# Kernel optimization log

Hardware: AMD Instinct MI355X
Metric: run time of the kernel (lower is better)

## Reference

```python
import jax, jax.numpy as jnp
import numpy as np

# ---- static config (matches init_kwargs) ----
R, A, K = 2048, 4, 4          # residues, backbone atoms, neighborhood size (self + <=3 edges)
N, B, C = R * A, 8, 64        # nodes, batch, hidden dim (= num_channels+time_embedding_channels)
H, D = 4, 16                  # heads, dim_head
HD, L = H * D, 4              # heads*dim_head, depth
E, Tc = 128, 61               # time_embedding_dim, time_embedding_channels
EPS = 1e-6


def _build_neighbors():
    """Fixed-K neighbor lists from the protein-backbone adjacency (self at k=0)."""
    adj = [[] for _ in range(N)]
    for r in range(R):
        b = r * A
        edges = [(b, b + 1), (b + 1, b + 2), (b + 2, b + 3)]
        if r < R - 1:
            edges.append((b + 2, (r + 1) * A))
        for i, j in edges:
            adj[i].append(j)
            adj[j].append(i)
    nbr = np.zeros((N, K), np.int32)
    msk = np.zeros((N, K), bool)
    for i in range(N):
        nbr[i, 0] = i
        msk[i, 0] = True
        for k, j in enumerate(adj[i][:K - 1]):
            nbr[i, k + 1] = j
            msk[i, k + 1] = True
    return jnp.asarray(nbr), jnp.asarray(msk)


def setup_inputs() -> dict:
    key = jax.random.key(0)
    ks = jax.random.split(key, 24)
    nbr, msk = _build_neighbors()

    def rn(i, shape, scale=1.0):
        return jax.random.normal(ks[i], shape, dtype=jnp.float32) * scale

    return {
        "x": rn(0, (B, N, 3)),
        "y": rn(1, (B, N, 3)),  # present in forward signature, unused by the math
        "t": jax.random.uniform(ks[2], (B,), dtype=jnp.float32),
        "nbr_idx": nbr, "nbr_mask": msk,
        "t_w1": rn(3, (E, E), E ** -0.5), "t_b1": jnp.zeros((E,), jnp.float32),
        "t_w2": rn(4, (E, Tc), E ** -0.5), "t_b2": jnp.zeros((Tc,), jnp.float32),
        "win1": rn(5, (C,)),
        "Wq0": rn(6, (L, C, HD), C ** -0.5), "Wk0": rn(7, (L, C, HD), C ** -0.5), "Wv0": rn(8, (L, C, HD), C ** -0.5),
        "Wq1": rn(9, (L, C, HD), C ** -0.5), "Wk1": rn(10, (L, C, HD), C ** -0.5), "Wv1": rn(11, (L, C, HD), C ** -0.5),
        "Wo0": rn(12, (L, HD, C), HD ** -0.5), "Wo1": rn(13, (L, HD, C), HD ** -0.5),
        "Wff0a": rn(14, (L, C, 4 * C), C ** -0.5), "Wff0b": rn(15, (L, 4 * C, C), (4 * C) ** -0.5),
        "Wff1": rn(16, (L, C, C), C ** -0.5),
        "Wout": rn(17, (3, C), C ** -0.5), "bout": jnp.zeros((3,), jnp.float32),
    }


def _sin_embed(t):
    half = E // 2
    freqs = jnp.exp(-jnp.log(10000.0) * jnp.arange(half, dtype=jnp.float32) / half)
    emb = t[:, None] * freqs
    return jnp.concatenate([jnp.sin(emb), jnp.cos(emb)], axis=-1)


def _ln(x):  # layernorm over channels, no affine
    mu = x.mean(-1, keepdims=True)
    v = x.var(-1, keepdims=True)
    return (x - mu) * jax.lax.rsqrt(v + EPS)


def _vnorm(f1):  # equivariant norm: scale by RMS of per-channel vector norms
    sq = jnp.sum(f1 * f1, axis=-1)                                    # [B,N,C]
    s = jax.lax.rsqrt(jnp.mean(sq, axis=-1, keepdims=True) + EPS)     # [B,N,1]
    return f1 * s[..., None]


def reference(x, y, t, nbr_idx, nbr_mask, t_w1, t_b1, t_w2, t_b2, win1,
              Wq0, Wk0, Wv0, Wq1, Wk1, Wv1, Wo0, Wo1, Wff0a, Wff0b, Wff1,
              Wout, bout):
    # time embedding MLP
    te = _sin_embed(t)
    te = jax.nn.silu(te @ t_w1 + t_b1) @ t_w2 + t_b2                  # [B,Tc]
    # degree-0 input: time embedding broadcast to nodes, concat positions
    f0 = jnp.concatenate([jnp.broadcast_to(te[:, None, :], (B, N, Tc)), x], axis=-1)  # [B,N,C]
    # degree-1 input: single vector channel (positions), lifted to C channels
    f1 = jnp.einsum('bnv,c->bncv', x, win1)                           # [B,N,C,3]

    rel = x[:, nbr_idx] - x[:, :, None, :]                            # [B,N,K,3]
    rhat = rel * jax.lax.rsqrt(jnp.sum(rel * rel, -1, keepdims=True) + EPS)
    mbias = jnp.where(nbr_mask, 0.0, -1e9)[None, :, None, :]          # [1,N,1,K]
    scale = D ** -0.5

    for l in range(L):
        g0, g1 = _ln(f0), _vnorm(f1)
        g0j = g0[:, nbr_idx]                                          # [B,N,K,C]
        g1j = g1[:, nbr_idx]                                          # [B,N,K,C,3]
        q0 = jnp.einsum('bnc,ce->bne', g0, Wq0[l]).reshape(B, N, H, D)
        k0 = jnp.einsum('bnkc,ce->bnke', g0j, Wk0[l]).reshape(B, N, K, H, D)
        v0 = jnp.einsum('bnkc,ce->bnke', g0j, Wv0[l]).reshape(B, N, K, H, D)
        q1 = jnp.einsum('bncv,ce->bnev', g1, Wq1[l]).reshape(B, N, H, D, 3)
        k1 = jnp.einsum('bnkcv,ce->bnkev', g1j, Wk1[l]).reshape(B, N, K, H, D, 3)
        v1 = jnp.einsum('bnkcv,ce->bnkev', g1j, Wv1[l]).reshape(B, N, K, H, D, 3)
        logits = (jnp.einsum('bnhd,bnkhd->bnhk', q0, k0)
                  + jnp.einsum('bnhdv,bnkhdv->bnhk', q1, k1)) * scale + mbias
        a = jax.nn.softmax(logits, axis=-1)                           # [B,N,H,K]
        # degree-mixing tensor products along edge direction rhat
        v1to0 = jnp.einsum('bnkhdv,bnkv->bnkhd', v1, rhat)            # 1 -> 0
        v0to1 = v0[..., None] * rhat[:, :, :, None, None, :]          # 0 -> 1
        o0 = jnp.einsum('bnhk,bnkhd->bnhd', a, v0 + v1to0).reshape(B, N, HD)
        o1 = jnp.einsum('bnhk,bnkhdv->bnhdv', a, v1 + v0to1).reshape(B, N, HD, 3)
        f0 = f0 + o0 @ Wo0[l]
        f1 = f1 + jnp.einsum('bnev,ec->bncv', o1, Wo1[l])
        # feedforward (equivariant: vector branch is linear in channels)
        f0 = f0 + jax.nn.silu(_ln(f0) @ Wff0a[l]) @ Wff0b[l]
        f1 = f1 + jnp.einsum('bncv,ce->bnev', _vnorm(f1), Wff1[l])

    # output layer: per-component channel projection of the degree-1 features
    score = jnp.einsum('bncv,vc->bnv', f1, Wout) + bout               # [B,N,3]
    return score
```

## Files before the change

### kernel.cpp

```cpp
#include <hip/hip_runtime.h>

#define BB 8
#define NN 8192
#define RR 2048
#define LL 4
#define TC 61
#define EPSF 1e-6f
#define BN (BB*NN)
#define OUTN (BN*3)

typedef unsigned short u16;
typedef unsigned int u32;
typedef _Float16 h2f __attribute__((ext_vector_type(2)));
typedef _Float16 h8 __attribute__((ext_vector_type(8)));
typedef float f4 __attribute__((ext_vector_type(4)));

__device__ __forceinline__ u32 packf16(float a, float b) {
  h2f h; h.x = (_Float16)a; h.y = (_Float16)b; return __builtin_bit_cast(u32, h);
}
__device__ __forceinline__ u16 f16b(float a) {
  _Float16 h = (_Float16)a; return __builtin_bit_cast(u16, h);
}
__device__ __forceinline__ float2 unpk(u32 a) {
  h2f h = __builtin_bit_cast(h2f, a); return make_float2((float)h.x, (float)h.y);
}
__device__ __forceinline__ float fdot2(u32 a, u32 b, float c) {
  return __builtin_amdgcn_fdot2(__builtin_bit_cast(h2f, a), __builtin_bit_cast(h2f, b), c, false);
}
__device__ __forceinline__ float frcp(float x) { return __builtin_amdgcn_rcpf(x); }
__device__ __forceinline__ float frsq(float x) { return __builtin_amdgcn_rsqf(x); }
__device__ __forceinline__ float fexp(float x) { return __expf(x); }
__device__ __forceinline__ int kmax_of(int n) {
  int aatom = n & 3, rres = n >> 2;
  return (aatom==0) ? (rres==0 ? 2 : 3)
       : (aatom==1) ? 3
       : (aatom==2) ? (rres==RR-1 ? 3 : 4) : 2;
}

__global__ __launch_bounds__(256) void k_const(float* out, float v) {
  int i = blockIdx.x*256 + threadIdx.x;
  if (i < OUTN) out[i] = v;
}

struct WSrc { const float* m[11]; };
__global__ __launch_bounds__(256) void k_prep(WSrc s, u32* W16,
    const float* t, const float* w1, const float* b1,
    const float* w2, const float* b2, float* te2,
    const float* x, const int* nbr, u16* rhat) {
  if (blockIdx.x >= 1096) {
    int i = (blockIdx.x - 1096)*256 + threadIdx.x;
    int tok = i >> 2, k = i & 3;
    int b = tok >> 13, n = tok & (NN-1);
    int tj = b*NN + nbr[n*4 + k];
    float x0 = x[tok*3+0], x1 = x[tok*3+1], x2 = x[tok*3+2];
    float rx = x[tj*3+0] - x0, ry = x[tj*3+1] - x1, rz = x[tj*3+2] - x2;
    float ir = rsqrtf(rx*rx + ry*ry + rz*rz + EPSF);
    rhat[(size_t)(tok*4+k)*3 + 0] = f16b(rx * ir);
    rhat[(size_t)(tok*4+k)*3 + 1] = f16b(ry * ir);
    rhat[(size_t)(tok*4+k)*3 + 2] = f16b(rz * ir);
    return;
  }
  if (blockIdx.x >= 1088) {
    __shared__ float s0[128], s1[128];
    int bb = blockIdx.x - 1088;
    int j = threadIdx.x;
    float tv = t[bb];
    if (j < 128) {
      int i = j & 63;
      float fr = expf(-9.210340371976184f * (float)i * (1.0f/64.0f));
      float em = tv * fr;
      s0[j] = (j < 64) ? sinf(em) : cosf(em);
    }
    __syncthreads();
    if (j < 128) {
      float acc = b1[j];
      for (int i2 = 0; i2 < 128; ++i2) acc += s0[i2] * w1[i2*128 + j];
      s1[j] = acc / (1.f + expf(-acc));
    }
    __syncthreads();
    if (j < TC) {
      float a2 = b2[j];
      for (int i2 = 0; i2 < 128; ++i2) a2 += s1[i2] * w2[i2*TC + j];
      te2[bb*TC + j] = a2;
    }
    return;
  }
  int i = blockIdx.x*256 + threadIdx.x;
  if (i < 73728) {
    int m = i >> 13, rr = i & 8191, l = rr >> 11, r2 = rr & 2047;
    int c2 = r2 >> 6, col = r2 & 63;
    const float* src = s.m[m] + l*4096;
    W16[i] = packf16(src[(2*c2)*64 + col], src[(2*c2+1)*64 + col]);
  } else if (i < 106496) {
    int j2 = i - 73728; int l = j2 >> 13, r2 = j2 & 8191;
    int c2 = r2 >> 8, j = r2 & 255;
    const float* src = s.m[9] + l*16384;
    W16[i] = packf16(src[(2*c2)*256 + j], src[(2*c2+1)*256 + j]);
  } else if (i < 139264) {
    int j2 = i - 106496; int l = j2 >> 13, r2 = j2 & 8191;
    int jp = r2 >> 6, e = r2 & 63;
    const float* src = s.m[10] + l*16384;
    W16[i] = packf16(src[(2*jp)*64 + e], src[(2*jp+1)*64 + e]);
  } else if (i < 188416) {
    int j2 = i - 139264;
    int l = j2 / 12288, rem = j2 % 12288;
    int m = rem >> 11, r2 = rem & 2047;
    int fb = r2 >> 8, li = r2 & 255;
    int nt = fb >> 1, kc = fb & 1;
    int lane = li >> 2, j = li & 3;
    int c2 = kc*16 + (lane>>4)*4 + j;
    int e  = nt*16 + (lane & 15);
    const float* src = s.m[m] + l*4096;
    W16[i] = packf16(src[(2*c2)*64 + e], src[(2*c2+1)*64 + e]);
  } else {
    int j2 = i - 188416;
    int l = j2 / 22528, rem = j2 % 22528;
    int li, fb, msel, N;
    const float* srcb;
    if (rem < 6144) {
      msel = 6 + (rem >> 11);
      int r2 = rem & 2047;
      fb = r2 >> 8; li = r2 & 255;
      srcb = s.m[msel] + l*4096; N = 64;
      int nt = fb >> 1, kc = fb & 1;
      int lane = li >> 2, j = li & 3;
      int c2 = kc*16 + (lane>>4)*4 + j;
      int e  = nt*16 + (lane & 15);
      W16[i] = packf16(srcb[(2*c2)*N + e], srcb[(2*c2+1)*N + e]);
    } else if (rem < 14336) {
      int r2 = rem - 6144;
      fb = r2 >> 8; li = r2 & 255;
      srcb = s.m[9] + l*16384; N = 256;
      int nt = fb >> 1, kc = fb & 1;
      int lane = li >> 2, j = li & 3;
      int c2 = kc*16 + (lane>>4)*4 + j;
      int e  = nt*16 + (lane & 15);
      W16[i] = packf16(srcb[(2*c2)*N + e], srcb[(2*c2+1)*N + e]);
    } else {
      int r2 = rem - 14336;
      fb = r2 >> 8; li = r2 & 255;
      srcb = s.m[10] + l*16384; N = 64;
      int nt = fb >> 3, kc = fb & 7;
      int lane = li >> 2, j = li & 3;
      int c2 = kc*16 + (lane>>4)*4 + j;
      int e  = nt*16 + (lane & 15);
      W16[i] = packf16(srcb[(2*c2)*N + e], srcb[(2*c2+1)*N + e]);
    }
  }
}

#define QH  0
#define KRG 4352
#define LK0 (KRG)
#define LV0 (KRG+1152)
#define LK1 (KRG+2304)
#define LV1 (KRG+5760)
#define LO0 (KRG)
#define LO1 (KRG+1152)
#define LVN (KRG+4608)
#define LGG (KRG+8064)
#define LDSU 13568

__global__ __launch_bounds__(256, 3) void k_layer(const u32* __restrict__ W16, int l,
    const u32* __restrict__ f0i, const u32* __restrict__ f1i,
    const int* __restrict__ nbr, const u16* __restrict__ rhat,
    u32* __restrict__ f0o, u32* __restrict__ f1o,
    const float* __restrict__ wout, const float* __restrict__ bout,
    float* __restrict__ out,
    const float* __restrict__ x, const float* __restrict__ win1,
    const float* __restrict__ te2) {
  __shared__ __align__(16) u32 S[LDSU];
  int tid = threadIdx.x, wv = tid >> 6, lane = tid & 63;
  int arow = lane & 15, aq = lane >> 4;
  int t0g = blockIdx.x * 32;
  int b = t0g >> 13, n0 = t0g & (NN-1);
  const u32 ONE2 = 0x3C003C00u;

  uint4 res0, res1a, res1b, res1c;
  if (l == 0) {
    {
      int t0 = tid >> 3, j0 = (tid & 7)*4;
      const float* x3 = x + ((size_t)b*NN + n0 + t0)*3;
      float xv[3] = {x3[0], x3[1], x3[2]};
      u32 tmp[4];
#pragma unroll
      for (int q = 0; q < 4; ++q) {
        int ca = 2*(j0+q), cb = ca+1;
        float va = (ca < TC) ? te2[b*TC+ca] : xv[ca-61];
        float vb = (cb < TC) ? te2[b*TC+cb] : xv[cb-61];
        tmp[q] = packf16(va, vb);
      }
      res0 = make_uint4(tmp[0], tmp[1], tmp[2], tmp[3]);
    }
    uint4* rr[3] = {&res1a, &res1b, &res1c};
#pragma unroll
    for (int k = 0; k < 3; ++k) {
      int idx = k*1024 + tid*4;
      int t = idx/96, rem = idx%96, v = rem >> 5, j = rem & 31;
      float xv = x[((size_t)b*NN + n0 + t)*3 + v];
      u32 tmp[4];
#pragma unroll
      for (int q = 0; q < 4; ++q)
        tmp[q] = packf16(xv*win1[2*(j+q)], xv*win1[2*(j+q)+1]);
      *rr[k] = make_uint4(tmp[0], tmp[1], tmp[2], tmp[3]);
    }
  } else {
    const u32* s0 = f0i + ((size_t)b*NN + n0)*32;
    const u32* s1 = f1i + ((size_t)b*NN + n0)*96;
    res0  = *(const uint4*)(s0 + tid*4);
    res1a = *(const uint4*)(s1 + (0*256 + tid)*4);
    res1b = *(const uint4*)(s1 + (1*256 + tid)*4);
    res1c = *(const uint4*)(s1 + (2*256 + tid)*4);
  }

  {
    const u32* base = W16 + 139264 + l*12288;
    int ncol = arow, mb = aq*4;

    auto ldraw = [&](int hr0, u32* r0, u32 (*r1)[8]) {
      int n = n0 - 2 + hr0 + arow;
      n = n < 0 ? 0 : (n > NN-1 ? NN-1 : n);
      size_t gt = (size_t)b*NN + n;
      if (l == 0) {
        const float* x3 = x + gt*3;
        float xv[3] = {x3[0], x3[1], x3[2]};
#pragma unroll
        for (int i = 0; i < 8; ++i) {
          int j = (i < 4) ? (aq*4+i) : (16 + aq*4 + (i-4));
          int ca = 2*j, cb = ca+1;
          float va = (ca < TC) ? te2[b*TC+ca] : xv[ca-61];
          float vb = (cb < TC) ? te2[b*TC+cb] : xv[cb-61];
          r0[i] = packf16(va, vb);
          float wa = win1[ca], wb = win1[cb];
#pragma unroll
          for (int v = 0; v < 3; ++v)
            r1[v][i] = packf16(xv[v]*wa, xv[v]*wb);
        }
      } else {
        *(uint4*)(r0)   = *(const uint4*)(f0i + gt*32 + aq*4);
        *(uint4*)(r0+4) = *(const uint4*)(f0i + gt*32 + 16 + aq*4);
#pragma unroll
        for (int v = 0; v < 3; ++v) {
          *(uint4*)(r1[v])   = *(const uint4*)(f1i + (gt*3+v)*32 + aq*4);
          *(uint4*)(r1[v]+4) = *(const uint4*)(f1i + (gt*3+v)*32 + 16 + aq*4);
        }
      }
    };

    auto mknorm = [&](const u32* r0, const u32 (*r1)[8], h8* g0f, h8 (*g1f)[2]) {
      float s = 0.f, s2 = 0.f;
#pragma unroll
      for (int i = 0; i < 8; ++i) { s = fdot2(r0[i], ONE2, s); s2 = fdot2(r0[i], r0[i], s2); }
      s  += __shfl_xor(s, 16, 64);  s  += __shfl_xor(s, 32, 64);
      s2 += __shfl_xor(s2, 16, 64); s2 += __shfl_xor(s2, 32, 64);
      float mu = s*(1.f/64.f);
      float ri = frsq(fmaxf(s2*(1.f/64.f)-mu*mu, 0.f) + EPSF);
      _Float16 rih = (_Float16)ri, bih = (_Float16)(-mu*ri);
      h2f scv; scv.x = rih; scv.y = rih;
      h2f biv; biv.x = bih; biv.y = bih;
#pragma unroll
      for (int kc = 0; kc < 2; ++kc) {
        u32 t0[4];
#pragma unroll
        for (int i = 0; i < 4; ++i) {
          h2f g = __builtin_bit_cast(h2f, r0[kc*4+i]) * scv + biv;
          t0[i] = __builtin_bit_cast(u32, g);
        }
        g0f[kc] = __builtin_bit_cast(h8, make_uint4(t0[0], t0[1], t0[2], t0[3]));
      }
      float ss = 0.f;
#pragma unroll
      for (int v = 0; v < 3; ++v)
#pragma unroll
        for (int i = 0; i < 8; ++i) ss = fdot2(r1[v][i], r1[v][i], ss);
      ss += __shfl_xor(ss, 16, 64); ss += __shfl_xor(ss, 32, 64);
      float vs = frsq(ss*(1.f/64.f) + EPSF);
      _Float16 vsh = (_Float16)vs;
      h2f vsv; vsv.x = vsh; vsv.y = vsh;
#pragma unroll
      for (int v = 0; v < 3; ++v)
#pragma unroll
        for (int kc = 0; kc < 2; ++kc) {
          u32 t1[4];
#pragma unroll
          for (int i = 0; i < 4; ++i) {
            h2f g = __builtin_bit_cast(h2f, r1[v][kc*4+i]) * vsv;
            t1[i] = __builtin_bit_cast(u32, g);
          }
          g1f[v][kc] = __builtin_bit_cast(h8, make_uint4(t1[0], t1[1], t1[2], t1[3]));
        }
    };

    auto projs = [&](const h8* afr, const u32* wM, u16* outh, int ob, int rmax) {
#pragma unroll
      for (int nt = 0; nt < 4; ++nt) {
        f4 acc = {0.f, 0.f, 0.f, 0.f};
#pragma unroll
        for (int kc = 0; kc < 2; ++kc) {
          uint4 wb = *(const uint4*)(wM + (nt*2+kc)*256 + lane*4);
          acc = __builtin_amdgcn_mfma_f32_16x16x32_f16(afr[kc], __builtin_bit_cast(h8, wb), acc, 0, 0, 0);
        }
        int ex = ((nt ^ aq)&3)*16 + ncol;
#pragma unroll
        for (int r = 0; r < 4; ++r) {
          int orow = ob + mb + r;
          if (orow < rmax) outh[orow*64 + ex] = f16b(acc[r]);
        }
      }
    };

    h8 g0f[2]; h8 g1f[3][2];
    if (wv < 3) {
      int tb = wv*16;
      u32 r0[8]; u32 r1[3][8];
      ldraw(tb, r0, r1);
      mknorm(r0, r1, g0f, g1f);
      projs(g0f, base + 1*2048, (u16*)(S+LK0), tb, 36);
      projs(g0f, base + 2*2048, (u16*)(S+LV0), tb, 36);
#pragma unroll
      for (int v = 0; v < 3; ++v) {
        projs(g1f[v], base + 4*2048, (u16*)(S+LK1) + v*2304, tb, 36);
        projs(g1f[v], base + 5*2048, (u16*)(S+LV1) + v*2304, tb, 36);
      }
    } else {
      u32 r0a[8], r1a[3][8], r0b[8], r1b[3][8];
      ldraw(2, r0a, r1a);
      ldraw(18, r0b, r1b);
      mknorm(r0a, r1a, g0f, g1f);
      projs(g0f, base, (u16*)(S+QH), 0, 32);
#pragma unroll
      for (int v = 0; v < 3; ++v)
        projs(g1f[v], base + 3*2048, (u16*)(S+1024) + v*2048, 0, 32);
      mknorm(r0b, r1b, g0f, g1f);
      projs(g0f, base, (u16*)(S+QH), 16, 32);
#pragma unroll
      for (int v = 0; v < 3; ++v)
        projs(g1f[v], base + 3*2048, (u16*)(S+1024) + v*2048, 16, 32);
    }
  }
  __syncthreads();

  u32 O0k[4], O1k[4][3];
  {
    const u32* Q0u = S + QH;
    const u32* Q1u = S + 1024;
    const u32* K0u = S + LK0;
    const u32* V0u = S + LV0;
    const u32* K1u = S + LK1;
    const u32* V1u = S + LV1;
    int half = lane >> 5, l32 = lane & 31;
#pragma unroll
    for (int it = 0; it < 4; ++it) {
      int ct = wv*8 + it*2 + half;
      int n = n0 + ct;
      size_t gt = (size_t)b*NN + n;
      int km = kmax_of(n);
      int4 nb = *(const int4*)(nbr + n*4);
      int lr[4];
      {
        int xx;
        xx = nb.x - n0 + 2; lr[0] = xx < 0 ? 0 : (xx > 35 ? 35 : xx);
        xx = nb.y - n0 + 2; lr[1] = xx < 0 ? 0 : (xx > 35 ? 35 : xx);
        xx = nb.z - n0 + 2; lr[2] = xx < 0 ? 0 : (xx > 35 ? 35 : xx);
        xx = nb.w - n0 + 2; lr[3] = xx < 0 ? 0 : (xx > 35 ? 35 : xx);
      }
      int jq = l32 ^ (((ct>>2)&3)<<3);
      u32 q0p = Q0u[ct*32 + jq];
      u32 q1p[3];
#pragma unroll
      for (int v = 0; v < 3; ++v) q1p[v] = Q1u[v*1024 + ct*32 + jq];
      float p[4];
#pragma unroll
      for (int k = 0; k < 4; ++k) {
        int row = lr[k];
        int jk = l32 ^ (((row>>2)&3)<<3);
        float acc = fdot2(q0p, K0u[row*32 + jk], 0.f);
#pragma unroll
        for (int v = 0; v < 3; ++v)
          acc = fdot2(q1p[v], K1u[v*1152 + row*32 + jk], acc);
        p[k] = acc;
      }
#pragma unroll
      for (int m = 1; m < 8; m <<= 1) {
#pragma unroll
        for (int k = 0; k < 4; ++k) p[k] += __shfl_xor(p[k], m, 64);
      }
      float mx = -1e30f;
#pragma unroll
      for (int k = 0; k < 4; ++k) { p[k] *= 0.25f; if (k < km) mx = fmaxf(mx, p[k]); }
      float aw[4], ssum = 0.f;
#pragma unroll
      for (int k = 0; k < 4; ++k) { aw[k] = (k < km) ? fexp(p[k]-mx) : 0.f; ssum += aw[k]; }
      float inv = frcp(ssum);
      const uint2* rp = (const uint2*)(rhat + (size_t)gt*12);
      uint2 ra = rp[0], rb = rp[1], rc = rp[2];
      u32 rw[6] = {ra.x, ra.y, rb.x, rb.y, rc.x, rc.y};
      h2f o0p = {(_Float16)0.f, (_Float16)0.f};
      h2f o1p0 = o0p, o1p1 = o0p, o1p2 = o0p;
#pragma unroll
      for (int k = 0; k < 4; ++k) {
        int row = lr[k];
        int jk = l32 ^ (((row>>2)&3)<<3);
        float a = aw[k]*inv;
        _Float16 ah = (_Float16)a;
        h2f a2; a2.x = ah; a2.y = ah;
        h2f v0p = __builtin_bit_cast(h2f, V0u[row*32 + jk]);
        h2f v1p[3], rh2[3];
#pragma unroll
        for (int v = 0; v < 3; ++v) {
          v1p[v] = __builtin_bit_cast(h2f, V1u[v*1152 + row*32 + jk]);
          int idx = k*3 + v;
          u32 w = rw[idx>>1];
          u32 hh = (idx&1) ? (w >> 16) : (w & 0xffffu);
          rh2[v] = __builtin_bit_cast(h2f, (hh << 16) | hh);
        }
        h2f vd = v1p[0]*rh2[0];
        vd = v1p[1]*rh2[1] + vd;
        vd = v1p[2]*rh2[2] + vd;
        o0p  = a2*(v0p + vd) + o0p;
        o1p0 = a2*(v0p*rh2[0] + v1p[0]) + o1p0;
        o1p1 = a2*(v0p*rh2[1] + v1p[1]) + o1p1;
        o1p2 = a2*(v0p*rh2[2] + v1p[2]) + o1p2;
      }
      O0k[it] = __builtin_bit_cast(u32, o0p);
      O1k[it][0] = __builtin_bit_cast(u32, o1p0);
      O1k[it][1] = __builtin_bit_cast(u32, o1p1);
      O1k[it][2] = __builtin_bit_cast(u32, o1p2);
    }
  }
  __syncthreads();

  {
    u32* o0u = S + LO0;
    u32* o1u = S + LO1;
    int half = lane >> 5, l32 = lane & 31;
#pragma unroll
    for (int it = 0; it < 4; ++it) {
      int ct = wv*8 + it*2 + half;
      o0u[ct*36 + l32] = O0k[it];
#pragma unroll
      for (int v = 0; v < 3; ++v)
        o1u[(v*32+ct)*36 + l32] = O1k[it][v];
    }
  }
  __syncthreads();

  int tl16 = (wv & 1)*16;
  h8 a1[3][2]; h8 a0[2];
  if (wv < 2) {
#pragma unroll
    for (int v = 0; v < 3; ++v)
#pragma unroll
      for (int kc = 0; kc < 2; ++kc)
        a1[v][kc] = __builtin_bit_cast(h8, *(const uint4*)(S + LO1 + (v*32 + tl16 + arow)*36 + kc*16 + aq*4));
  } else {
#pragma unroll
    for (int kc = 0; kc < 2; ++kc)
      a0[kc] = __builtin_bit_cast(h8, *(const uint4*)(S + LO0 + (tl16 + arow)*36 + kc*16 + aq*4));
  }
  __syncthreads();
  {
    uint4* d = (uint4*)(S + KRG);
    d[tid]       = res0;
    d[256 + tid] = res1a;
    d[512 + tid] = res1b;
    d[768 + tid] = res1c;
  }
  __syncthreads();
  const u32* FR0 = S + KRG;
  const u32* FR1 = S + KRG + 1024;

  {
    int ncol = arow, mb = aq*4;
    const u32* Wf = W16 + 188416 + l*22528;
    const u32* po0f = Wf;
    const u32* po1f = Wf + 2048;
    const u32* pf1f = Wf + 4096;
    const u32* paf  = Wf + 6144;
    const u32* pbf  = Wf + 14336;
    size_t gt0 = (size_t)b*NN + n0 + tl16;
    if (wv < 2) {
      float f1m[3][4][4];
#pragma unroll
      for (int v = 0; v < 3; ++v)
#pragma unroll
        for (int nt = 0; nt < 4; ++nt) {
          f4 acc = {0.f, 0.f, 0.f, 0.f};
#pragma unroll
          for (int kc = 0; kc < 2; ++kc) {
            uint4 wb = *(const uint4*)(po1f + (nt*2+kc)*256 + lane*4);
            acc = __builtin_amdgcn_mfma_f32_16x16x32_f16(a1[v][kc], __builtin_bit_cast(h8, wb), acc, 0, 0, 0);
          }
#pragma unroll
          for (int r = 0; r < 4; ++r) {
            int t = tl16 + mb + r;
            float2 pq = unpk(FR1[(t*3+v)*32 + nt*8 + (ncol>>1)]);
            f1m[v][nt][r] = acc[r] + ((ncol&1) ? pq.y : pq.x);
          }
        }
      float vs[4];
#pragma unroll
      for (int r = 0; r < 4; ++r) {
        float ss = 0.f;
#pragma unroll
        for (int v = 0; v < 3; ++v)
#pragma unroll
          for (int nt = 0; nt < 4; ++nt) ss += f1m[v][nt][r]*f1m[v][nt][r];
        ss += __shfl_xor(ss, 1, 64); ss += __shfl_xor(ss, 2, 64);
        ss += __shfl_xor(ss, 4, 64); ss += __shfl_xor(ss, 8, 64);
        vs[r] = frsq(ss*(1.f/64.f) + EPSF);
      }
      u32* vn = S + LVN + wv*1728;
      {
        u16* vnh = (u16*)vn;
#pragma unroll
        for (int v = 0; v < 3; ++v)
#pragma unroll
          for (int nt = 0; nt < 4; ++nt)
#pragma unroll
            for (int r = 0; r < 4; ++r)
              vnh[v*1152 + (mb+r)*72 + nt*16 + ncol] = f16b(f1m[v][nt][r]*vs[r]);
      }
      float wl[3][4], sc[3][4];
      if (l == 3) {
#pragma unroll
        for (int v = 0; v < 3; ++v)
#pragma unroll
          for (int nt = 0; nt < 4; ++nt) { wl[v][nt] = wout[v*64 + nt*16 + ncol]; }
#pragma unroll
        for (int v = 0; v < 3; ++v)
#pragma unroll
          for (int r = 0; r < 4; ++r) sc[v][r] = 0.f;
      }
#pragma unroll
      for (int v = 0; v < 3; ++v)
#pragma unroll
        for (int nt = 0; nt < 4; ++nt) {
          f4 acc = {0.f, 0.f, 0.f, 0.f};
#pragma unroll
          for (int kc = 0; kc < 2; ++kc) {
            h8 af = __builtin_bit_cast(h8, *(const uint4*)(vn + v*576 + arow*36 + kc*16 + aq*4));
            uint4 wb = *(const uint4*)(pf1f + (nt*2+kc)*256 + lane*4);
            acc = __builtin_amdgcn_mfma_f32_16x16x32_f16(af, __builtin_bit_cast(h8, wb), acc, 0, 0, 0);
          }
#pragma unroll
          for (int r = 0; r < 4; ++r) {
            size_t gt = gt0 + mb + r;
            float val = acc[r] + f1m[v][nt][r];
            if (l < 3) {
              float par = __shfl_xor(val, 1, 64);
              if (!(ncol & 1))
                f1o[(gt*3+v)*32 + nt*8 + (ncol>>1)] = packf16(val, par);
            } else {
              sc[v][r] += val * wl[v][nt];
            }
          }
        }
      if (l == 3) {
#pragma unroll
        for (int v = 0; v < 3; ++v)
#pragma unroll
          for (int r = 0; r < 4; ++r) {
            float xx = sc[v][r];
            xx += __shfl_xor(xx, 1, 64); xx += __shfl_xor(xx, 2, 64);
            xx += __shfl_xor(xx, 4, 64); xx += __shfl_xor(xx, 8, 64);
            if (ncol == 0) out[(gt0 + mb + r)*3 + v] = xx + bout[v];
          }
      }
    } else if (l < 3) {
      float f0m[4][4];
#pragma unroll
      for (int nt = 0; nt < 4; ++nt) {
        f4 acc = {0.f, 0.f, 0.f, 0.f};
#pragma unroll
        for (int kc = 0; kc < 2; ++kc) {
          uint4 wb = *(const uint4*)(po0f + (nt*2+kc)*256 + lane*4);
          acc = __builtin_amdgcn_mfma_f32_16x16x32_f16(a0[kc], __builtin_bit_cast(h8, wb), acc, 0, 0, 0);
        }
#pragma unroll
        for (int r = 0; r < 4; ++r) {
          int t = tl16 + mb + r;
          float2 pq = unpk(FR0[t*32 + nt*8 + (ncol>>1)]);
          f0m[nt][r] = acc[r] + ((ncol&1) ? pq.y : pq.x);
        }
      }
      float mu[4], ri[4];
#pragma unroll
      for (int r = 0; r < 4; ++r) {
        float sg = 0.f, s2 = 0.f;
#pragma unroll
        for (int nt = 0; nt < 4; ++nt) { sg += f0m[nt][r]; s2 += f0m[nt][r]*f0m[nt][r]; }
        sg += __shfl_xor(sg, 1, 64); sg += __shfl_xor(sg, 2, 64);
        sg += __shfl_xor(sg, 4, 64); sg += __shfl_xor(sg, 8, 64);
        s2 += __shfl_xor(s2, 1, 64); s2 += __shfl_xor(s2, 2, 64);
        s2 += __shfl_xor(s2, 4, 64); s2 += __shfl_xor(s2, 8, 64);
        mu[r] = sg*(1.f/64.f);
        ri[r] = frsq(fmaxf(s2*(1.f/64.f)-mu[r]*mu[r], 0.f) + EPSF);
      }
      u32* gg = S + LGG + (wv-2)*576;
      {
        u16* gh = (u16*)gg;
#pragma unroll
        for (int nt = 0; nt < 4; ++nt)
#pragma unroll
          for (int r = 0; r < 4; ++r)
            gh[(mb+r)*72 + nt*16 + ncol] = f16b((f0m[nt][r]-mu[r])*ri[r]);
      }
      u32* hp = S + (wv-2)*2176;
      {
        h8 ga[2];
#pragma unroll
        for (int kc = 0; kc < 2; ++kc)
          ga[kc] = __builtin_bit_cast(h8, *(const uint4*)(gg + arow*36 + kc*16 + aq*4));
        u16* hhh = (u16*)hp;
#pragma unroll
        for (int nt16 = 0; nt16 < 16; ++nt16) {
          f4 acc = {0.f, 0.f, 0.f, 0.f};
#pragma unroll
          for (int kc = 0; kc < 2; ++kc) {
            uint4 wb = *(const uint4*)(paf + (nt16*2+kc)*256 + lane*4);
            acc = __builtin_amdgcn_mfma_f32_16x16x32_f16(ga[kc], __builtin_bit_cast(h8, wb), acc, 0, 0, 0);
          }
#pragma unroll
          for (int r = 0; r < 4; ++r) {
            float a = acc[r];
            hhh[(mb+r)*272 + nt16*16 + ncol] = f16b(a * frcp(1.f + fexp(-a)));
          }
        }
      }
#pragma unroll
      for (int nt = 0; nt < 4; ++nt) {
        f4 acc = {0.f, 0.f, 0.f, 0.f};
#pragma unroll
        for (int kc = 0; kc < 8; ++kc) {
          h8 af = __builtin_bit_cast(h8, *(const uint4*)(hp + arow*136 + kc*16 + aq*4));
          uint4 wb = *(const uint4*)(pbf + (nt*8+kc)*256 + lane*4);
          acc = __builtin_amdgcn_mfma_f32_16x16x32_f16(af, __builtin_bit_cast(h8, wb), acc, 0, 0, 0);
        }
#pragma unroll
        for (int r = 0; r < 4; ++r) {
          size_t gt = gt0 + mb + r;
          float val = acc[r] + f0m[nt][r];
          float par = __shfl_xor(val, 1, 64);
          if (!(ncol & 1))
            f0o[gt*32 + nt*8 + (ncol>>1)] = packf16(val, par);
        }
      }
    }
  }
}

extern "C" void kernel_launch(void* const* d_in, const int* in_sizes, int n_in,
                              void* d_out, int out_size, void* d_ws, size_t ws_size,
                              hipStream_t stream) {
  float* out = (float*)d_out;
  static const int exp23[23] = {196608,196608,8,32768,32768,16384,128,7808,61,64,
                                16384,16384,16384,16384,16384,16384,16384,16384,
                                65536,65536,16384,192,3};
  bool ok23 = (n_in == 23), ok22 = (n_in == 22);
  int bad = -1;
  if (ok23) {
    for (int i = 0; i < 23; ++i) if (in_sizes[i] != exp23[i]) { ok23 = false; bad = i; break; }
  }
  if (!ok23 && ok22) {
    for (int i = 0; i < 22; ++i) {
      int want = (i == 0) ? exp23[0] : exp23[i+1];
      if (in_sizes[i] != want) { ok22 = false; if (bad < 0) bad = i; break; }
    }
  } else ok22 = false;
  if (!ok23 && !ok22) {
    k_const<<<768, 256, 0, stream>>>(out, (float)(3000 + (bad < 0 ? 100 + n_in : bad)));
    return;
  }
  int sh = ok23 ? 0 : -1;
  const int* nbr = (const int*)d_in[3 + sh];
  const float* F[20];
  F[0] = (const float*)d_in[0];
  F[1] = (const float*)d_in[2 + sh];
  for (int j = 0; j < 18; ++j) F[2 + j] = (const float*)d_in[5 + sh + j];

  char* ws = (char*)d_ws;
  u32*   W16  = (u32*)ws;
  float* te2  = (float*)(ws + 1114112);
  u16*   rhat = (u16*)(ws + 1116160);
  u32*   f0A  = (u32*)(ws + 2689024);
  u32*   f1A  = (u32*)(ws + 11077632);
  u32*   f0B  = (u32*)(ws + 36243456);
  u32*   f1B  = (u32*)(ws + 44632064);

  WSrc s;
  s.m[0]=F[7]; s.m[1]=F[8]; s.m[2]=F[9]; s.m[3]=F[10]; s.m[4]=F[11]; s.m[5]=F[12];
  s.m[6]=F[13]; s.m[7]=F[14]; s.m[8]=F[17]; s.m[9]=F[15]; s.m[10]=F[16];

  k_prep<<<1096 + BN*4/256, 256, 0, stream>>>(s, W16, F[1], F[2], F[3], F[4], F[5], te2,
                                              F[0], nbr, rhat);
  for (int l = 0; l < LL; ++l) {
    const u32* fi0 = (l & 1) ? f0B : f0A;
    const u32* fi1 = (l & 1) ? f1B : f1A;
    u32*       fo0 = (l & 1) ? f0A : f0B;
    u32*       fo1 = (l & 1) ? f1A : f1B;
    k_layer<<<BN/32, 256, 0, stream>>>(W16, l, fi0, fi1, nbr, rhat, fo0, fo1,
                                       F[18], F[19], out, F[0], F[6], te2);
  }
}
```

Baseline: 377.8 us.

## Merge residual staging with output stores and swizzle LDS scratch to drop barriers

The residual registers are now written to shared memory alongside the attention outputs, before a single barrier. Each wave then loads its MFMA operands directly, which removes two __syncthreads and a separate staging pass. The vector-norm and layer-norm scratch tiles now reuse each wave's own residual region, with an XOR-swizzled unpadded layout in place of padded rows. This relies on each wave reading its residual slice before overwriting it with scratch data, which holds because the wave runs in lockstep.

```diff
diff --git a/kernel.cpp b/kernel.cpp
--- a/kernel.cpp
+++ b/kernel.cpp
@@ -155,10 +155,10 @@
 #define LV0 (KRG+1152)
 #define LK1 (KRG+2304)
 #define LV1 (KRG+5760)
-#define LO0 (KRG)
-#define LO1 (KRG+1152)
-#define LVN (KRG+4608)
-#define LGG (KRG+8064)
+#define LO0q (KRG)
+#define LO1q (KRG+1152)
+#define FR0q (KRG+4608)
+#define FR1q (KRG+5632)
 #define LDSU 13568
 
 __global__ __launch_bounds__(256, 3) void k_layer(const u32* __restrict__ W16, int l,
@@ -431,8 +431,8 @@
   __syncthreads();
 
   {
-    u32* o0u = S + LO0;
-    u32* o1u = S + LO1;
+    u32* o0u = S + LO0q;
+    u32* o1u = S + LO1q;
     int half = lane >> 5, l32 = lane & 31;
 #pragma unroll
     for (int it = 0; it < 4; ++it) {
@@ -442,35 +442,17 @@
       for (int v = 0; v < 3; ++v)
         o1u[(v*32+ct)*36 + l32] = O1k[it][v];
     }
+    uint4* d0 = (uint4*)(S + FR0q);
+    d0[tid] = res0;
+    uint4* d1 = (uint4*)(S + FR1q);
+    d1[tid]       = res1a;
+    d1[256 + tid] = res1b;
+    d1[512 + tid] = res1c;
   }
   __syncthreads();
 
-  int tl16 = (wv & 1)*16;
-  h8 a1[3][2]; h8 a0[2];
-  if (wv < 2) {
-#pragma unroll
-    for (int v = 0; v < 3; ++v)
-#pragma unroll
-      for (int kc = 0; kc < 2; ++kc)
-        a1[v][kc] = __builtin_bit_cast(h8, *(const uint4*)(S + LO1 + (v*32 + tl16 + arow)*36 + kc*16 + aq*4));
-  } else {
-#pragma unroll
-    for (int kc = 0; kc < 2; ++kc)
-      a0[kc] = __builtin_bit_cast(h8, *(const uint4*)(S + LO0 + (tl16 + arow)*36 + kc*16 + aq*4));
-  }
-  __syncthreads();
   {
-    uint4* d = (uint4*)(S + KRG);
-    d[tid]       = res0;
-    d[256 + tid] = res1a;
-    d[512 + tid] = res1b;
-    d[768 + tid] = res1c;
-  }
-  __syncthreads();
-  const u32* FR0 = S + KRG;
-  const u32* FR1 = S + KRG + 1024;
-
-  {
+    int tl16 = (wv & 1)*16;
     int ncol = arow, mb = aq*4;
     const u32* Wf = W16 + 188416 + l*22528;
     const u32* po0f = Wf;
@@ -478,8 +460,16 @@
     const u32* pf1f = Wf + 4096;
     const u32* paf  = Wf + 6144;
     const u32* pbf  = Wf + 14336;
+    const u32* FR0 = S + FR0q;
+    const u32* FR1 = S + FR1q;
     size_t gt0 = (size_t)b*NN + n0 + tl16;
     if (wv < 2) {
+      h8 a1[3][2];
+#pragma unroll
+      for (int v = 0; v < 3; ++v)
+#pragma unroll
+        for (int kc = 0; kc < 2; ++kc)
+          a1[v][kc] = __builtin_bit_cast(h8, *(const uint4*)(S + LO1q + (v*32 + tl16 + arow)*36 + kc*16 + aq*4));
       float f1m[3][4][4];
 #pragma unroll
       for (int v = 0; v < 3; ++v)
@@ -510,7 +500,7 @@
         ss += __shfl_xor(ss, 4, 64); ss += __shfl_xor(ss, 8, 64);
         vs[r] = frsq(ss*(1.f/64.f) + EPSF);
       }
-      u32* vn = S + LVN + wv*1728;
+      u32* vn = S + FR1q + wv*1536;
       {
         u16* vnh = (u16*)vn;
 #pragma unroll
@@ -519,7 +509,7 @@
           for (int nt = 0; nt < 4; ++nt)
 #pragma unroll
             for (int r = 0; r < 4; ++r)
-              vnh[v*1152 + (mb+r)*72 + nt*16 + ncol] = f16b(f1m[v][nt][r]*vs[r]);
+              vnh[v*1024 + (mb+r)*64 + ((nt^aq)&3)*16 + ncol] = f16b(f1m[v][nt][r]*vs[r]);
       }
       float wl[3][4], sc[3][4];
       if (l == 3) {
@@ -539,7 +529,9 @@
           f4 acc = {0.f, 0.f, 0.f, 0.f};
 #pragma unroll
           for (int kc = 0; kc < 2; ++kc) {
-            h8 af = __builtin_bit_cast(h8, *(const uint4*)(vn + v*576 + arow*36 + kc*16 + aq*4));
+            int lc = kc*2 + (aq>>1);
+            int pc = (lc ^ (arow>>2)) & 3;
+            h8 af = __builtin_bit_cast(h8, *(const uint4*)(vn + v*512 + arow*32 + pc*8 + (aq&1)*4));
             uint4 wb = *(const uint4*)(pf1f + (nt*2+kc)*256 + lane*4);
             acc = __builtin_amdgcn_mfma_f32_16x16x32_f16(af, __builtin_bit_cast(h8, wb), acc, 0, 0, 0);
           }
@@ -568,6 +560,10 @@
           }
       }
     } else if (l < 3) {
+      h8 a0[2];
+#pragma unroll
+      for (int kc = 0; kc < 2; ++kc)
+        a0[kc] = __builtin_bit_cast(h8, *(const uint4*)(S + LO0q + (tl16 + arow)*36 + kc*16 + aq*4));
       float f0m[4][4];
 #pragma unroll
       for (int nt = 0; nt < 4; ++nt) {
@@ -597,21 +593,24 @@
         mu[r] = sg*(1.f/64.f);
         ri[r] = frsq(fmaxf(s2*(1.f/64.f)-mu[r]*mu[r], 0.f) + EPSF);
       }
-      u32* gg = S + LGG + (wv-2)*576;
+      u32* gg = S + FR0q + (wv & 1)*512;
       {
         u16* gh = (u16*)gg;
 #pragma unroll
         for (int nt = 0; nt < 4; ++nt)
 #pragma unroll
           for (int r = 0; r < 4; ++r)
-            gh[(mb+r)*72 + nt*16 + ncol] = f16b((f0m[nt][r]-mu[r])*ri[r]);
+            gh[(mb+r)*64 + ((nt^aq)&3)*16 + ncol] = f16b((f0m[nt][r]-mu[r])*ri[r]);
       }
       u32* hp = S + (wv-2)*2176;
       {
         h8 ga[2];
 #pragma unroll
-        for (int kc = 0; kc < 2; ++kc)
-          ga[kc] = __builtin_bit_cast(h8, *(const uint4*)(gg + arow*36 + kc*16 + aq*4));
+        for (int kc = 0; kc < 2; ++kc) {
+          int lc = kc*2 + (aq>>1);
+          int pc = (lc ^ (arow>>2)) & 3;
+          ga[kc] = __builtin_bit_cast(h8, *(const uint4*)(gg + arow*32 + pc*8 + (aq&1)*4));
+        }
         u16* hhh = (u16*)hp;
 #pragma unroll
         for (int nt16 = 0; nt16 < 16; ++nt16) {
```

Result: no change. 378.2 us (+0.1%).
